# Performance work log

Measured on AMD Instinct MI355X. Metric: run time of the kernel, lower is better.

The kernel has to match this reference:

```python
import jax, jax.numpy as jnp
import numpy as np

EMBED_DIM = 1024
NUM_HEADS = 16
HEAD_DIM = EMBED_DIM // NUM_HEADS
B, S = 2, 2048


def setup_inputs() -> dict:
    key = jax.random.key(0)
    ks = jax.random.split(key, 11)
    glorot = lambda k, shape: jax.random.normal(k, shape, jnp.float32) * (2.0 / sum(shape)) ** 0.5
    return {
        "query": jax.random.normal(ks[0], (B, S, EMBED_DIM), jnp.float32),
        "key": jax.random.normal(ks[1], (B, S, EMBED_DIM), jnp.float32),
        "value": jax.random.normal(ks[2], (B, S, EMBED_DIM), jnp.float32),
        "Wq": glorot(ks[3], (EMBED_DIM, EMBED_DIM)), "bq": jnp.zeros((EMBED_DIM,), jnp.float32),
        "Wk": glorot(ks[4], (EMBED_DIM, EMBED_DIM)), "bk": jnp.zeros((EMBED_DIM,), jnp.float32),
        "Wv": glorot(ks[5], (EMBED_DIM, EMBED_DIM)), "bv": jnp.zeros((EMBED_DIM,), jnp.float32),
        "Wo": glorot(ks[6], (EMBED_DIM, EMBED_DIM)), "bo": jnp.zeros((EMBED_DIM,), jnp.float32),
    }


def reference(query, key, value, Wq, bq, Wk, bk, Wv, bv, Wo, bo):
    b, s, _ = query.shape
    # QKV projections
    q = query @ Wq + bq
    k = key @ Wk + bk
    v = value @ Wv + bv
    # [B, S, H, D] -> [B, H, S, D]
    q = q.reshape(b, s, NUM_HEADS, HEAD_DIM).transpose(0, 2, 1, 3)
    k = k.reshape(b, s, NUM_HEADS, HEAD_DIM).transpose(0, 2, 1, 3)
    v = v.reshape(b, s, NUM_HEADS, HEAD_DIM).transpose(0, 2, 1, 3)
    # scores [B, H, S, S], materialized as in the original
    scores = jnp.einsum("bhqd,bhkd->bhqk", q, k) / jnp.sqrt(jnp.float32(HEAD_DIM))
    attn = jax.nn.softmax(scores, axis=-1)
    out = jnp.einsum("bhqk,bhkd->bhqd", attn, v)  # [B, H, S, D]
    out = out.transpose(0, 2, 1, 3).reshape(b, s, EMBED_DIM)
    return out @ Wo + bo
```

## Files before the change

kernel.cpp:

```cpp
#include <hip/hip_runtime.h>
#include <hip/hip_bf16.h>


#define EMBED 1024
#define NHEAD 16
#define HDIM 64
#define SEQ 2048
#define MROWS 4096

typedef __attribute__((ext_vector_type(8))) __bf16 bf16x8;
typedef __attribute__((ext_vector_type(4))) float f32x4;
typedef __attribute__((ext_vector_type(16))) float f32x16;

__device__ __forceinline__ unsigned short f2bf(float f) {
  unsigned int u = __builtin_bit_cast(unsigned int, f);
  u += 0x7fffu + ((u >> 16) & 1u);
  return (unsigned short)(u >> 16);
}

__device__ __forceinline__ int cvtpk_bf16(float lo, float hi) {
  int r;
  asm("v_cvt_pk_bf16_f32 %0, %1, %2" : "=v"(r) : "v"(lo), "v"(hi));
  return r;
}

__device__ __forceinline__ float max3f(float a, float b, float c) {
  return fmaxf(fmaxf(a, b), c);
}

__device__ __forceinline__ int swz(int row, int bcol) {
  return row * 128 + (bcol ^ ((row & 7) << 4));
}

__device__ __forceinline__ void gload16(const void* g, void* l) {
  __builtin_amdgcn_global_load_lds((const __attribute__((address_space(1))) void*)g,
                                   (__attribute__((address_space(3))) void*)l, 16, 0, 0);
}

__global__ __launch_bounds__(256) void prep(const float* __restrict__ q32, const float* __restrict__ k32,
                                            const float* __restrict__ v32,
                                            unsigned short* __restrict__ Xq, unsigned short* __restrict__ Xk,
                                            unsigned short* __restrict__ Xv,
                                            const float* __restrict__ w0, const float* __restrict__ w1,
                                            const float* __restrict__ w2, const float* __restrict__ w3,
                                            unsigned short* __restrict__ o0, unsigned short* __restrict__ o1,
                                            unsigned short* __restrict__ o2, unsigned short* __restrict__ o3) {
  __shared__ float tile[64][65];
  const int id = blockIdx.x;
  if (id < 6144) {
    const float* in; unsigned short* out;
    switch (id >> 11) {
      case 0: in = q32; out = Xq; break;
      case 1: in = k32; out = Xk; break;
      default: in = v32; out = Xv; break;
    }
    int i = (id & 2047) * 256 + threadIdx.x;
    const float4* p = reinterpret_cast<const float4*>(in) + (size_t)i * 2;
    float4 a = p[0], b = p[1];
    int4 r;
    r.x = cvtpk_bf16(a.x, a.y);
    r.y = cvtpk_bf16(a.z, a.w);
    r.z = cvtpk_bf16(b.x, b.y);
    r.w = cvtpk_bf16(b.z, b.w);
    reinterpret_cast<int4*>(out)[i] = r;
  } else {
    const int wid = id - 6144;
    const float* src; unsigned short* dst;
    switch (wid >> 8) {
      case 0: src = w0; dst = o0; break;
      case 1: src = w1; dst = o1; break;
      case 2: src = w2; dst = o2; break;
      default: src = w3; dst = o3; break;
    }
    const int k0 = ((wid >> 4) & 15) * 64, n0 = (wid & 15) * 64;
    const int c = threadIdx.x & 63, r0 = threadIdx.x >> 6;
#pragma unroll
    for (int i = 0; i < 16; ++i) {
      int r = r0 + i * 4;
      tile[r][c] = src[(size_t)(k0 + r) * EMBED + n0 + c];
    }
    __syncthreads();
#pragma unroll
    for (int i = 0; i < 16; ++i) {
      int nr = r0 + i * 4;
      dst[(size_t)(n0 + nr) * EMBED + k0 + c] = f2bf(tile[c][nr]);
    }
  }
}

template <int BN>
__device__ __forceinline__ void gemm_core(const unsigned short* __restrict__ A,
                                          const unsigned short* __restrict__ Bt,
                                          const float* __restrict__ bias,
                                          void* __restrict__ C, float oscale, int mode,
                                          int m0, int n0) {
  constexpr int K = EMBED;
  constexpr int MF = (BN == 128) ? 4 : 2;
  constexpr int BRW = BN / 4;
  __shared__ __align__(16) unsigned short Alds[128 * 64];
  __shared__ __align__(16) unsigned short Blds[BN * 64];
  char* Ab8 = (char*)Alds; char* Bb8 = (char*)Blds;
  const char* AB = (const char*)A;
  const char* BB = (const char*)Bt;
  const int tid = threadIdx.x;
  const int lane = tid & 63, w = tid >> 6;
  const int wr = (BN == 128) ? (w >> 1) : w;
  const int wc = (BN == 128) ? (w & 1) : 0;
  const int fr = lane & 15, fq = lane >> 4;
  const int bcol = (lane & 7) * 16;
  const int gsc = bcol ^ ((lane >> 3) << 4);

  f32x4 acc[MF][4];
#pragma unroll
  for (int m = 0; m < MF; ++m)
#pragma unroll
    for (int n = 0; n < 4; ++n) acc[m][n] = f32x4{0.f, 0.f, 0.f, 0.f};

#define GSTAGE(k0_)                                                                          \
  {                                                                                          \
    _Pragma("unroll") for (int i_ = 0; i_ < 4; ++i_) {                                       \
      int row_ = w * 32 + i_ * 8 + (lane >> 3);                                              \
      gload16(AB + (size_t)(m0 + row_) * (K * 2) + (k0_)*2 + gsc, Ab8 + w * 4096 + i_ * 1024); \
    }                                                                                        \
    _Pragma("unroll") for (int i_ = 0; i_ < BRW / 8; ++i_) {                                 \
      int row_ = w * BRW + i_ * 8 + (lane >> 3);                                             \
      gload16(BB + (size_t)(n0 + row_) * (K * 2) + (k0_)*2 + gsc,                            \
              Bb8 + w * (BRW * 128) + i_ * 1024);                                            \
    }                                                                                        \
  }

  GSTAGE(0);

  for (int k0 = 0; k0 < K; k0 += 64) {
    __syncthreads();
    bf16x8 af2[2][MF], bf2[2][4];
#pragma unroll
    for (int ks = 0; ks < 2; ++ks) {
#pragma unroll
      for (int m = 0; m < MF; ++m) {
        int ar = wr * (MF * 16) + m * 16 + fr;
        af2[ks][m] = *reinterpret_cast<const bf16x8*>(Ab8 + swz(ar, ks * 64 + fq * 16));
      }
#pragma unroll
      for (int n = 0; n < 4; ++n) {
        int br = wc * 64 + n * 16 + fr;
        bf2[ks][n] = *reinterpret_cast<const bf16x8*>(Bb8 + swz(br, ks * 64 + fq * 16));
      }
    }
    __syncthreads();
    if (k0 + 64 < K) GSTAGE(k0 + 64);
#pragma unroll
    for (int ks = 0; ks < 2; ++ks)
#pragma unroll
      for (int m = 0; m < MF; ++m)
#pragma unroll
        for (int n = 0; n < 4; ++n)
          acc[m][n] = __builtin_amdgcn_mfma_f32_16x16x32_bf16(af2[ks][m], bf2[ks][n], acc[m][n], 0, 0, 0);
  }
#undef GSTAGE

#pragma unroll
  for (int n = 0; n < 4; ++n) {
    int col = n0 + wc * 64 + n * 16 + fr;
    float bv = bias[col];
#pragma unroll
    for (int m = 0; m < MF; ++m) {
      int rowb = m0 + wr * (MF * 16) + m * 16 + fq * 4;
      if (mode == 2) {
        int b = rowb >> 11, s0 = rowb & (SEQ - 1);
        int s0p = (s0 & ~12) | ((s0 & 4) << 1) | ((s0 & 8) >> 1);
        int h = col >> 6, d = col & 63;
        int2 pk;
        pk.x = cvtpk_bf16((acc[m][n][0] + bv) * oscale, (acc[m][n][1] + bv) * oscale);
        pk.y = cvtpk_bf16((acc[m][n][2] + bv) * oscale, (acc[m][n][3] + bv) * oscale);
        *reinterpret_cast<int2*>(
            &reinterpret_cast<unsigned short*>(C)[((size_t)((b * NHEAD + h) * HDIM + d)) * SEQ + s0p]) = pk;
      } else if (mode == 0) {
#pragma unroll
        for (int r = 0; r < 4; ++r) {
          int row = rowb + r;
          float v = (acc[m][n][r] + bv) * oscale;
          int b = row >> 11, s = row & (SEQ - 1), h = col >> 6, d = col & 63;
          reinterpret_cast<unsigned short*>(C)[((size_t)((b * NHEAD + h) * SEQ + s) << 6) + d] = f2bf(v);
        }
      } else {
#pragma unroll
        for (int r = 0; r < 4; ++r)
          reinterpret_cast<float*>(C)[(size_t)(rowb + r) * EMBED + col] = acc[m][n][r] + bv;
      }
    }
  }
}

__global__ __launch_bounds__(256) void gemm_qkv(
    const unsigned short* __restrict__ Xq, const unsigned short* __restrict__ Xk,
    const unsigned short* __restrict__ Xv,
    const unsigned short* __restrict__ Wqt, const unsigned short* __restrict__ Wkt,
    const unsigned short* __restrict__ Wvt,
    const float* __restrict__ bq, const float* __restrict__ bk, const float* __restrict__ bv,
    unsigned short* __restrict__ Qb, unsigned short* __restrict__ Kb,
    unsigned short* __restrict__ Vtb, float qscale) {
  const int id = blockIdx.x;
  const int lg = (id & 7) * 96 + (id >> 3);
  const int z = lg >> 8, rem = lg & 255;
  const int m0 = (rem >> 3) * 128, n0 = (rem & 7) * 128;
  switch (z) {
    case 0: gemm_core<128>(Xq, Wqt, bq, Qb, qscale, 0, m0, n0); break;
    case 1: gemm_core<128>(Xk, Wkt, bk, Kb, 1.0f, 0, m0, n0); break;
    default: gemm_core<128>(Xv, Wvt, bv, Vtb, 1.0f, 2, m0, n0); break;
  }
}

__global__ __launch_bounds__(256) void gemm_out(const unsigned short* __restrict__ A,
                                                const unsigned short* __restrict__ Bt,
                                                const float* __restrict__ bias,
                                                float* __restrict__ C) {
  const int id = blockIdx.x;
  const int lg = (id & 7) * 64 + (id >> 3);
  const int m0 = (lg >> 4) * 128, n0 = (lg & 15) * 64;
  gemm_core<64>(A, Bt, bias, C, 1.0f, 1, m0, n0);
}

__global__ __launch_bounds__(128) void attn(const unsigned short* __restrict__ Q,
                                            const unsigned short* __restrict__ Kk,
                                            const unsigned short* __restrict__ Vt,
                                            unsigned short* __restrict__ AO) {
  __shared__ __align__(16) unsigned short Klds[2][64 * 64];
  __shared__ __align__(16) unsigned short Vlds[2][64 * 64];
  const int tid = threadIdx.x, lane = tid & 63, w = tid >> 6;
  const int ql = lane & 31, t = lane >> 5;

  const int lin = blockIdx.x;
  const int head = (lin & 7) * 4 + ((lin >> 3) & 3);
  const int q0 = (lin >> 5) * 64;
  const size_t hb = (size_t)head * SEQ * HDIM;
  const unsigned short* Qh = Q + hb;
  const char* KhB = (const char*)(Kk + hb);
  const char* VhB = (const char*)(Vt + hb);

  const int gsc = ((lane & 7) * 16) ^ ((lane >> 3) << 4);
  const int row0 = w * 32 + (lane >> 3);

#define STAGE(kt_, b_)                                                                     \
  {                                                                                        \
    char* kb_ = (char*)Klds[b_];                                                           \
    char* vb_ = (char*)Vlds[b_];                                                           \
    _Pragma("unroll") for (int i_ = 0; i_ < 4; ++i_) {                                     \
      gload16(KhB + (size_t)((kt_)*64 + row0 + i_ * 8) * 128 + gsc,                        \
              kb_ + w * 4096 + i_ * 1024);                                                 \
      gload16(VhB + (size_t)(row0 + i_ * 8) * (SEQ * 2) + (kt_)*128 + gsc,                 \
              vb_ + w * 4096 + i_ * 1024);                                                 \
    }                                                                                      \
  }

  bf16x8 qf[4];
  {
    const unsigned short* qp = Qh + (size_t)(q0 + w * 32 + ql) * HDIM + t * 8;
    qf[0] = *reinterpret_cast<const bf16x8*>(qp);
    qf[1] = *reinterpret_cast<const bf16x8*>(qp + 16);
    qf[2] = *reinterpret_cast<const bf16x8*>(qp + 32);
    qf[3] = *reinterpret_cast<const bf16x8*>(qp + 48);
  }
  f32x16 oacc0 = {}, oacc1 = {};
  float mrow = -1e30f, lrow = 0.f;

  STAGE(0, 0);
  __syncthreads();

  for (int kt = 0; kt < SEQ / 64; ++kt) {
    const int cur = kt & 1;
    const bool more = (kt + 1 < SEQ / 64);
    if (more) STAGE(kt + 1, cur ^ 1);
    char* Kb8 = (char*)Klds[cur];
    char* Vb8 = (char*)Vlds[cur];

    f32x16 sc0 = {}, sc1 = {};
    __builtin_amdgcn_s_setprio(1);
#pragma unroll
    for (int s = 0; s < 4; ++s) {
      bf16x8 kf0 = *reinterpret_cast<const bf16x8*>(Kb8 + swz(ql, s * 32 + t * 16));
      bf16x8 kf1 = *reinterpret_cast<const bf16x8*>(Kb8 + swz(32 + ql, s * 32 + t * 16));
      sc0 = __builtin_amdgcn_mfma_f32_32x32x16_bf16(kf0, qf[s], sc0, 0, 0, 0);
      sc1 = __builtin_amdgcn_mfma_f32_32x32x16_bf16(kf1, qf[s], sc1, 0, 0, 0);
    }
    __builtin_amdgcn_s_setprio(0);

    float l1[12];
#pragma unroll
    for (int i = 0; i < 5; ++i) l1[i] = max3f(sc0[3 * i], sc0[3 * i + 1], sc0[3 * i + 2]);
#pragma unroll
    for (int i = 0; i < 5; ++i) l1[5 + i] = max3f(sc1[3 * i], sc1[3 * i + 1], sc1[3 * i + 2]);
    l1[10] = sc0[15];
    l1[11] = sc1[15];
    float l2a = max3f(l1[0], l1[1], l1[2]);
    float l2b = max3f(l1[3], l1[4], l1[5]);
    float l2c = max3f(l1[6], l1[7], l1[8]);
    float l2d = max3f(l1[9], l1[10], l1[11]);
    float mt = fmaxf(max3f(l2a, l2b, l2c), l2d);
    mt = fmaxf(mt, __shfl_xor(mt, 32));

    if (!__all(mt <= mrow + 8.0f)) {
      float mn = fmaxf(mrow, mt);
      float resc = __builtin_amdgcn_exp2f(mrow - mn);
      lrow *= resc;
#pragma unroll
      for (int r = 0; r < 16; ++r) {
        float rq = __shfl(resc, (r & 3) + 8 * (r >> 2) + 4 * t, 64);
        oacc0[r] *= rq;
        oacc1[r] *= rq;
      }
      mrow = mn;
    }

    float ps0 = 0.f, ps1 = 0.f, ps2 = 0.f, ps3 = 0.f;
#pragma unroll
    for (int i = 0; i < 4; ++i) {
      sc0[4 * i + 0] = __builtin_amdgcn_exp2f(sc0[4 * i + 0] - mrow);
      sc0[4 * i + 1] = __builtin_amdgcn_exp2f(sc0[4 * i + 1] - mrow);
      sc0[4 * i + 2] = __builtin_amdgcn_exp2f(sc0[4 * i + 2] - mrow);
      sc0[4 * i + 3] = __builtin_amdgcn_exp2f(sc0[4 * i + 3] - mrow);
      sc1[4 * i + 0] = __builtin_amdgcn_exp2f(sc1[4 * i + 0] - mrow);
      sc1[4 * i + 1] = __builtin_amdgcn_exp2f(sc1[4 * i + 1] - mrow);
      sc1[4 * i + 2] = __builtin_amdgcn_exp2f(sc1[4 * i + 2] - mrow);
      sc1[4 * i + 3] = __builtin_amdgcn_exp2f(sc1[4 * i + 3] - mrow);
      ps0 += sc0[4 * i + 0] + sc0[4 * i + 1];
      ps1 += sc0[4 * i + 2] + sc0[4 * i + 3];
      ps2 += sc1[4 * i + 0] + sc1[4 * i + 1];
      ps3 += sc1[4 * i + 2] + sc1[4 * i + 3];
    }
    lrow += (ps0 + ps1) + (ps2 + ps3);

    int4 paw[4];
#pragma unroll
    for (int s2 = 0; s2 < 2; ++s2) {
      paw[s2].x     = cvtpk_bf16(sc0[8 * s2 + 0], sc0[8 * s2 + 1]);
      paw[s2].y     = cvtpk_bf16(sc0[8 * s2 + 2], sc0[8 * s2 + 3]);
      paw[s2].z     = cvtpk_bf16(sc0[8 * s2 + 4], sc0[8 * s2 + 5]);
      paw[s2].w     = cvtpk_bf16(sc0[8 * s2 + 6], sc0[8 * s2 + 7]);
      paw[2 + s2].x = cvtpk_bf16(sc1[8 * s2 + 0], sc1[8 * s2 + 1]);
      paw[2 + s2].y = cvtpk_bf16(sc1[8 * s2 + 2], sc1[8 * s2 + 3]);
      paw[2 + s2].z = cvtpk_bf16(sc1[8 * s2 + 4], sc1[8 * s2 + 5]);
      paw[2 + s2].w = cvtpk_bf16(sc1[8 * s2 + 6], sc1[8 * s2 + 7]);
    }

    __builtin_amdgcn_s_setprio(1);
#pragma unroll
    for (int s = 0; s < 4; ++s) {
      bf16x8 pa = __builtin_bit_cast(bf16x8, paw[s]);
      bf16x8 v0 = *reinterpret_cast<const bf16x8*>(Vb8 + swz(ql, s * 32 + t * 16));
      bf16x8 v1 = *reinterpret_cast<const bf16x8*>(Vb8 + swz(32 + ql, s * 32 + t * 16));
      oacc0 = __builtin_amdgcn_mfma_f32_32x32x16_bf16(pa, v0, oacc0, 0, 0, 0);
      oacc1 = __builtin_amdgcn_mfma_f32_32x32x16_bf16(pa, v1, oacc1, 0, 0, 0);
    }
    __builtin_amdgcn_s_setprio(0);

    __syncthreads();
  }
#undef STAGE

  lrow += __shfl_xor(lrow, 32);

  const int b = head >> 4, hh = head & 15;
#pragma unroll
  for (int r = 0; r < 16; ++r) {
    int qr = (r & 3) + 8 * (r >> 2) + 4 * t;
    float inv = 1.0f / __shfl(lrow, qr, 64);
    int srow = q0 + w * 32 + qr;
    size_t ob = (size_t)(b * SEQ + srow) * EMBED + hh * 64 + ql;
    AO[ob] = f2bf(oacc0[r] * inv);
    AO[ob + 32] = f2bf(oacc1[r] * inv);
  }
}

extern "C" void kernel_launch(void* const* d_in, const int* in_sizes, int n_in,
                              void* d_out, int out_size, void* d_ws, size_t ws_size,
                              hipStream_t stream) {
  const float* q32 = (const float*)d_in[0];
  const float* k32 = (const float*)d_in[1];
  const float* v32 = (const float*)d_in[2];
  const float* Wq = (const float*)d_in[3]; const float* bq = (const float*)d_in[4];
  const float* Wk = (const float*)d_in[5]; const float* bk = (const float*)d_in[6];
  const float* Wv = (const float*)d_in[7]; const float* bv = (const float*)d_in[8];
  const float* Wo = (const float*)d_in[9]; const float* bo = (const float*)d_in[10];
  float* out = (float*)d_out;

  char* ws = (char*)d_ws;
  const size_t MB = 1u << 20;
  unsigned short* Xq  = (unsigned short*)(ws + 0 * MB);
  unsigned short* Xk  = (unsigned short*)(ws + 8 * MB);
  unsigned short* Xv  = (unsigned short*)(ws + 16 * MB);
  unsigned short* Wqt = (unsigned short*)(ws + 24 * MB);
  unsigned short* Wkt = (unsigned short*)(ws + 26 * MB);
  unsigned short* Wvt = (unsigned short*)(ws + 28 * MB);
  unsigned short* Wot = (unsigned short*)(ws + 30 * MB);
  unsigned short* Qb  = (unsigned short*)(ws + 32 * MB);
  unsigned short* Kb  = (unsigned short*)(ws + 40 * MB);
  unsigned short* Vtb = (unsigned short*)(ws + 48 * MB);
  unsigned short* AO  = Xq;

  prep<<<7168, 256, 0, stream>>>(q32, k32, v32, Xq, Xk, Xv,
                                 Wq, Wk, Wv, Wo, Wqt, Wkt, Wvt, Wot);

  const float qscale = 0.125f * 1.44269504088896340736f;
  gemm_qkv<<<768, 256, 0, stream>>>(Xq, Xk, Xv, Wqt, Wkt, Wvt, bq, bk, bv,
                                    Qb, Kb, Vtb, qscale);

  attn<<<dim3(SEQ / 64 * 32), 128, 0, stream>>>(Qb, Kb, Vtb, AO);

  gemm_out<<<512, 256, 0, stream>>>(AO, Wot, bo, out);
}
```

Before: 124.1 us.

## Enlarge attention tiles to 128 queries and 128 keys per block with 4 waves

The attention kernel now runs 4 waves per block covering 128 query rows, and each loop iteration processes a 128-key tile instead of 64. The K/V staging loads and the LDS swizzles are rewritten for the wider tiles. The point is to share each staged K/V tile across more query rows and to halve the number of loop iterations and barriers. In exchange, LDS use per block and register pressure from four score accumulators go up, and the grid drops to 512 blocks, which may lower occupancy.

```diff
diff --git a/kernel.cpp b/kernel.cpp
--- a/kernel.cpp
+++ b/kernel.cpp
@@ -30,6 +30,9 @@
 
 __device__ __forceinline__ int swz(int row, int bcol) {
   return row * 128 + (bcol ^ ((row & 7) << 4));
+}
+__device__ __forceinline__ int swzv(int row, int bcol) {
+  return row * 256 + (bcol ^ ((row & 7) << 4));
 }
 
 __device__ __forceinline__ void gload16(const void* g, void* l) {
@@ -221,36 +224,37 @@
   gemm_core<64>(A, Bt, bias, C, 1.0f, 1, m0, n0);
 }
 
-__global__ __launch_bounds__(128) void attn(const unsigned short* __restrict__ Q,
+__global__ __launch_bounds__(256) void attn(const unsigned short* __restrict__ Q,
                                             const unsigned short* __restrict__ Kk,
                                             const unsigned short* __restrict__ Vt,
                                             unsigned short* __restrict__ AO) {
-  __shared__ __align__(16) unsigned short Klds[2][64 * 64];
-  __shared__ __align__(16) unsigned short Vlds[2][64 * 64];
+  __shared__ __align__(16) unsigned short Klds[2][128 * 64];
+  __shared__ __align__(16) unsigned short Vlds[2][64 * 128];
   const int tid = threadIdx.x, lane = tid & 63, w = tid >> 6;
   const int ql = lane & 31, t = lane >> 5;
 
   const int lin = blockIdx.x;
   const int head = (lin & 7) * 4 + ((lin >> 3) & 3);
-  const int q0 = (lin >> 5) * 64;
+  const int q0 = (lin >> 5) * 128;
   const size_t hb = (size_t)head * SEQ * HDIM;
   const unsigned short* Qh = Q + hb;
   const char* KhB = (const char*)(Kk + hb);
   const char* VhB = (const char*)(Vt + hb);
 
   const int gsc = ((lane & 7) * 16) ^ ((lane >> 3) << 4);
-  const int row0 = w * 32 + (lane >> 3);
-
-#define STAGE(kt_, b_)                                                                     \
-  {                                                                                        \
-    char* kb_ = (char*)Klds[b_];                                                           \
-    char* vb_ = (char*)Vlds[b_];                                                           \
-    _Pragma("unroll") for (int i_ = 0; i_ < 4; ++i_) {                                     \
-      gload16(KhB + (size_t)((kt_)*64 + row0 + i_ * 8) * 128 + gsc,                        \
-              kb_ + w * 4096 + i_ * 1024);                                                 \
-      gload16(VhB + (size_t)(row0 + i_ * 8) * (SEQ * 2) + (kt_)*128 + gsc,                 \
-              vb_ + w * 4096 + i_ * 1024);                                                 \
-    }                                                                                      \
+  const int gscv = ((lane & 15) * 16) ^ ((((w & 1) << 2) + (lane >> 4)) << 4);
+
+#define STAGE(kt_, b_)                                                                       \
+  {                                                                                          \
+    char* kb_ = (char*)Klds[b_];                                                             \
+    char* vb_ = (char*)Vlds[b_];                                                             \
+    _Pragma("unroll") for (int i_ = 0; i_ < 4; ++i_) {                                       \
+      int krow_ = i_ * 32 + w * 8 + (lane >> 3);                                             \
+      gload16(KhB + (size_t)((kt_)*128 + krow_) * 128 + gsc, kb_ + i_ * 4096 + tid * 16);    \
+      int vrow_ = i_ * 16 + w * 4 + (lane >> 4);                                             \
+      gload16(VhB + (size_t)vrow_ * (SEQ * 2) + (kt_)*256 + gscv,                            \
+              vb_ + i_ * 4096 + tid * 16);                                                   \
+    }                                                                                        \
   }
 
   bf16x8 qf[4];
@@ -267,36 +271,36 @@
   STAGE(0, 0);
   __syncthreads();
 
-  for (int kt = 0; kt < SEQ / 64; ++kt) {
+  for (int kt = 0; kt < SEQ / 128; ++kt) {
     const int cur = kt & 1;
-    const bool more = (kt + 1 < SEQ / 64);
+    const bool more = (kt + 1 < SEQ / 128);
     if (more) STAGE(kt + 1, cur ^ 1);
     char* Kb8 = (char*)Klds[cur];
     char* Vb8 = (char*)Vlds[cur];
 
-    f32x16 sc0 = {}, sc1 = {};
+    f32x16 sc[4] = {{}, {}, {}, {}};
     __builtin_amdgcn_s_setprio(1);
 #pragma unroll
     for (int s = 0; s < 4; ++s) {
-      bf16x8 kf0 = *reinterpret_cast<const bf16x8*>(Kb8 + swz(ql, s * 32 + t * 16));
-      bf16x8 kf1 = *reinterpret_cast<const bf16x8*>(Kb8 + swz(32 + ql, s * 32 + t * 16));
-      sc0 = __builtin_amdgcn_mfma_f32_32x32x16_bf16(kf0, qf[s], sc0, 0, 0, 0);
-      sc1 = __builtin_amdgcn_mfma_f32_32x32x16_bf16(kf1, qf[s], sc1, 0, 0, 0);
+#pragma unroll
+      for (int kb = 0; kb < 4; ++kb) {
+        bf16x8 kf = *reinterpret_cast<const bf16x8*>(Kb8 + swz(kb * 32 + ql, s * 32 + t * 16));
+        sc[kb] = __builtin_amdgcn_mfma_f32_32x32x16_bf16(kf, qf[s], sc[kb], 0, 0, 0);
+      }
     }
     __builtin_amdgcn_s_setprio(0);
 
-    float l1[12];
-#pragma unroll
-    for (int i = 0; i < 5; ++i) l1[i] = max3f(sc0[3 * i], sc0[3 * i + 1], sc0[3 * i + 2]);
-#pragma unroll
-    for (int i = 0; i < 5; ++i) l1[5 + i] = max3f(sc1[3 * i], sc1[3 * i + 1], sc1[3 * i + 2]);
-    l1[10] = sc0[15];
-    l1[11] = sc1[15];
-    float l2a = max3f(l1[0], l1[1], l1[2]);
-    float l2b = max3f(l1[3], l1[4], l1[5]);
-    float l2c = max3f(l1[6], l1[7], l1[8]);
-    float l2d = max3f(l1[9], l1[10], l1[11]);
-    float mt = fmaxf(max3f(l2a, l2b, l2c), l2d);
+    float mkb[4];
+#pragma unroll
+    for (int kb = 0; kb < 4; ++kb) {
+      float a = max3f(sc[kb][0], sc[kb][1], sc[kb][2]);
+      float b = max3f(sc[kb][3], sc[kb][4], sc[kb][5]);
+      float c = max3f(sc[kb][6], sc[kb][7], sc[kb][8]);
+      float d = max3f(sc[kb][9], sc[kb][10], sc[kb][11]);
+      float e = max3f(sc[kb][12], sc[kb][13], sc[kb][14]);
+      mkb[kb] = fmaxf(max3f(max3f(a, b, c), d, e), sc[kb][15]);
+    }
+    float mt = fmaxf(fmaxf(mkb[0], mkb[1]), fmaxf(mkb[2], mkb[3]));
     mt = fmaxf(mt, __shfl_xor(mt, 32));
 
     if (!__all(mt <= mrow + 8.0f)) {
@@ -312,43 +316,33 @@
       mrow = mn;
     }
 
+#pragma unroll
+    for (int kb = 0; kb < 4; ++kb)
+#pragma unroll
+      for (int i = 0; i < 16; ++i)
+        sc[kb][i] = __builtin_amdgcn_exp2f(sc[kb][i] - mrow);
     float ps0 = 0.f, ps1 = 0.f, ps2 = 0.f, ps3 = 0.f;
 #pragma unroll
-    for (int i = 0; i < 4; ++i) {
-      sc0[4 * i + 0] = __builtin_amdgcn_exp2f(sc0[4 * i + 0] - mrow);
-      sc0[4 * i + 1] = __builtin_amdgcn_exp2f(sc0[4 * i + 1] - mrow);
-      sc0[4 * i + 2] = __builtin_amdgcn_exp2f(sc0[4 * i + 2] - mrow);
-      sc0[4 * i + 3] = __builtin_amdgcn_exp2f(sc0[4 * i + 3] - mrow);
-      sc1[4 * i + 0] = __builtin_amdgcn_exp2f(sc1[4 * i + 0] - mrow);
-      sc1[4 * i + 1] = __builtin_amdgcn_exp2f(sc1[4 * i + 1] - mrow);
-      sc1[4 * i + 2] = __builtin_amdgcn_exp2f(sc1[4 * i + 2] - mrow);
-      sc1[4 * i + 3] = __builtin_amdgcn_exp2f(sc1[4 * i + 3] - mrow);
-      ps0 += sc0[4 * i + 0] + sc0[4 * i + 1];
-      ps1 += sc0[4 * i + 2] + sc0[4 * i + 3];
-      ps2 += sc1[4 * i + 0] + sc1[4 * i + 1];
-      ps3 += sc1[4 * i + 2] + sc1[4 * i + 3];
+    for (int i = 0; i < 8; ++i) {
+      ps0 += sc[0][2 * i] + sc[0][2 * i + 1];
+      ps1 += sc[1][2 * i] + sc[1][2 * i + 1];
+      ps2 += sc[2][2 * i] + sc[2][2 * i + 1];
+      ps3 += sc[3][2 * i] + sc[3][2 * i + 1];
     }
     lrow += (ps0 + ps1) + (ps2 + ps3);
 
-    int4 paw[4];
-#pragma unroll
-    for (int s2 = 0; s2 < 2; ++s2) {
-      paw[s2].x     = cvtpk_bf16(sc0[8 * s2 + 0], sc0[8 * s2 + 1]);
-      paw[s2].y     = cvtpk_bf16(sc0[8 * s2 + 2], sc0[8 * s2 + 3]);
-      paw[s2].z     = cvtpk_bf16(sc0[8 * s2 + 4], sc0[8 * s2 + 5]);
-      paw[s2].w     = cvtpk_bf16(sc0[8 * s2 + 6], sc0[8 * s2 + 7]);
-      paw[2 + s2].x = cvtpk_bf16(sc1[8 * s2 + 0], sc1[8 * s2 + 1]);
-      paw[2 + s2].y = cvtpk_bf16(sc1[8 * s2 + 2], sc1[8 * s2 + 3]);
-      paw[2 + s2].z = cvtpk_bf16(sc1[8 * s2 + 4], sc1[8 * s2 + 5]);
-      paw[2 + s2].w = cvtpk_bf16(sc1[8 * s2 + 6], sc1[8 * s2 + 7]);
-    }
-
     __builtin_amdgcn_s_setprio(1);
 #pragma unroll
-    for (int s = 0; s < 4; ++s) {
-      bf16x8 pa = __builtin_bit_cast(bf16x8, paw[s]);
-      bf16x8 v0 = *reinterpret_cast<const bf16x8*>(Vb8 + swz(ql, s * 32 + t * 16));
-      bf16x8 v1 = *reinterpret_cast<const bf16x8*>(Vb8 + swz(32 + ql, s * 32 + t * 16));
+    for (int s = 0; s < 8; ++s) {
+      const int kb = s >> 1, base = 8 * (s & 1);
+      int4 pw;
+      pw.x = cvtpk_bf16(sc[kb][base + 0], sc[kb][base + 1]);
+      pw.y = cvtpk_bf16(sc[kb][base + 2], sc[kb][base + 3]);
+      pw.z = cvtpk_bf16(sc[kb][base + 4], sc[kb][base + 5]);
+      pw.w = cvtpk_bf16(sc[kb][base + 6], sc[kb][base + 7]);
+      bf16x8 pa = __builtin_bit_cast(bf16x8, pw);
+      bf16x8 v0 = *reinterpret_cast<const bf16x8*>(Vb8 + swzv(ql, s * 32 + t * 16));
+      bf16x8 v1 = *reinterpret_cast<const bf16x8*>(Vb8 + swzv(32 + ql, s * 32 + t * 16));
       oacc0 = __builtin_amdgcn_mfma_f32_32x32x16_bf16(pa, v0, oacc0, 0, 0, 0);
       oacc1 = __builtin_amdgcn_mfma_f32_32x32x16_bf16(pa, v1, oacc1, 0, 0, 0);
     }
@@ -405,7 +399,7 @@
   gemm_qkv<<<768, 256, 0, stream>>>(Xq, Xk, Xv, Wqt, Wkt, Wvt, bq, bk, bv,
                                     Qb, Kb, Vtb, qscale);
 
-  attn<<<dim3(SEQ / 64 * 32), 128, 0, stream>>>(Qb, Kb, Vtb, AO);
+  attn<<<512, 256, 0, stream>>>(Qb, Kb, Vtb, AO);
 
   gemm_out<<<512, 256, 0, stream>>>(AO, Wot, bo, out);
 }
```

After: 132.5 us. 1.07x slower.
